# Performance work log

Hardware: AMD Instinct MI355X
Metric: run time of the kernel (lower is better)

## Reference

```python
import jax, jax.numpy as jnp
import numpy as np

N, E, F_IN, H, C = 50000, 800000, 50, 128, 121


def setup_inputs() -> dict:
    key = jax.random.key(0)
    ks = jax.random.split(key, 16)
    s = 0.05
    inp = {
        'x': jax.random.normal(ks[0], (N, F_IN), jnp.float32),
        'edge_index': jax.random.randint(ks[1], (2, E), 0, N, jnp.int64),
        'TRAIN': 0,
        'W1': jax.random.normal(ks[2], (F_IN, H), jnp.float32) * s,
        'b1': jnp.zeros((H,), jnp.float32),
        'W2': jax.random.normal(ks[3], (H, H), jnp.float32) * s,
        'b2': jnp.zeros((H,), jnp.float32),
        'W3': jax.random.normal(ks[4], (H, H), jnp.float32) * s,
        'b3': jnp.zeros((H,), jnp.float32),
        'fcW1': jax.random.normal(ks[5], (H, H), jnp.float32) * s,
        'fcb1': jnp.zeros((H,), jnp.float32),
        'fcW2': jax.random.normal(ks[6], (H, H), jnp.float32) * s,
        'fcb2': jnp.zeros((H,), jnp.float32),
        'fcW3': jax.random.normal(ks[7], (H, C), jnp.float32) * s,
        'fcb3': jnp.zeros((C,), jnp.float32),
    }
    return inp


def gcn_conv(x, W, b, src, dst, n):
    # PyG GCNConv: h = x @ W; symmetric norm with self-loops; aggregate at dst.
    h = x @ W
    deg = jax.ops.segment_sum(jnp.ones(src.shape[0], h.dtype), dst, num_segments=n) + 1.0
    dinv = jax.lax.rsqrt(deg)  # deg^{-1/2}, self-loop included
    norm = dinv[src] * dinv[dst]  # [E]
    agg = jax.ops.segment_sum(h[src] * norm[:, None], dst, num_segments=n)
    agg = agg + h * (dinv * dinv)[:, None]  # self-loop contribution
    return agg + b


def reference(x, edge_index, TRAIN, W1, b1, W2, b2, W3, b3, fcW1, fcb1, fcW2, fcb2, fcW3, fcb3):
    src, dst = edge_index[0], edge_index[1]
    n = x.shape[0]
    y = jax.nn.relu(gcn_conv(x, W1, b1, src, dst, n))
    y = jax.nn.relu(gcn_conv(y, W2, b2, src, dst, n))
    y = jax.nn.relu(gcn_conv(y, W3, b3, src, dst, n))
    y = jax.nn.relu(y @ fcW1 + fcb1)
    y = jax.nn.relu(y @ fcW2 + fcb2)
    y = y @ fcW3 + fcb3
    return y
```

## Files before the change

### kernel.cpp

```cpp
#include <hip/hip_runtime.h>

#define SCAN_CHUNK 2048

typedef short s16x8 __attribute__((ext_vector_type(8)));
typedef float f32x4 __attribute__((ext_vector_type(4)));

__device__ inline ushort f2b(float f) {
  uint u = __float_as_uint(f);
  return (ushort)((u + 0x7fffu + ((u >> 16) & 1u)) >> 16);
}
__device__ inline float b2f(uint h) { return __uint_as_float(h << 16); }

__global__ __launch_bounds__(256) void convert_hist_kernel(const void* __restrict__ ei,
                                                           int* __restrict__ src,
                                                           int* __restrict__ dst,
                                                           int* __restrict__ degi, int E) {
  __shared__ int sflag;
  if (threadIdx.x == 0) {
    const int* p32 = (const int*)ei;
    int is64 = 1;
#pragma unroll 4
    for (int i = 1; i < 256; i += 2)
      if (p32[i] != 0) { is64 = 0; break; }
    sflag = is64;
  }
  __syncthreads();
  int e = blockIdx.x * 256 + threadIdx.x;
  if (e >= E) return;
  int s, d;
  if (sflag) {
    const long long* p = (const long long*)ei;
    s = (int)p[e];
    d = (int)p[E + e];
  } else {
    const int* p = (const int*)ei;
    s = p[e];
    d = p[E + e];
  }
  src[e] = s;
  dst[e] = d;
  atomicAdd(&degi[d], 1);
}

__global__ __launch_bounds__(256) void chunk_reduce_kernel(const int* __restrict__ degi,
                                                           int* __restrict__ partials, int N) {
  __shared__ int s[256];
  int base = blockIdx.x * SCAN_CHUNK;
  int sum = 0;
  for (int j = 0; j < 8; ++j) {
    int i = base + threadIdx.x * 8 + j;
    if (i < N) sum += degi[i];
  }
  s[threadIdx.x] = sum;
  __syncthreads();
  for (int ofs = 128; ofs > 0; ofs >>= 1) {
    if ((int)threadIdx.x < ofs) s[threadIdx.x] += s[threadIdx.x + ofs];
    __syncthreads();
  }
  if (threadIdx.x == 0) partials[blockIdx.x] = s[0];
}

__global__ __launch_bounds__(256) void chunk_scan_kernel(int* __restrict__ degi,
                                                         const int* __restrict__ partials,
                                                         int nchunk,
                                                         int* __restrict__ rowptr,
                                                         float* __restrict__ dinv,
                                                         int N, int E) {
  __shared__ int s[256];
  __shared__ int sbase;
  int t = threadIdx.x;
  if (t == 0) {
    int acc = 0;
    for (int c = 0; c < (int)blockIdx.x; ++c) acc += partials[c];
    sbase = acc;
    if (blockIdx.x == 0) rowptr[N] = E;
  }
  int base = blockIdx.x * SCAN_CHUNK;
  int v[8];
  int tsum = 0;
  for (int j = 0; j < 8; ++j) {
    int i = base + t * 8 + j;
    v[j] = (i < N) ? degi[i] : 0;
    tsum += v[j];
  }
  s[t] = tsum;
  __syncthreads();
  for (int ofs = 1; ofs < 256; ofs <<= 1) {
    int add = (t >= ofs) ? s[t - ofs] : 0;
    __syncthreads();
    s[t] += add;
    __syncthreads();
  }
  int run = s[t] - tsum + sbase;
  for (int j = 0; j < 8; ++j) {
    int i = base + t * 8 + j;
    if (i < N) {
      rowptr[i] = run;
      dinv[i] = rsqrtf((float)v[j] + 1.0f);
      degi[i] = 0;
    }
    run += v[j];
  }
}

__global__ __launch_bounds__(256) void scatter_kernel(const int* __restrict__ src,
                                                      const int* __restrict__ dst,
                                                      const int* __restrict__ rowptr,
                                                      const float* __restrict__ dinv,
                                                      int* __restrict__ cnt,
                                                      uint* __restrict__ epack, int E, int N) {
  const int chunk = blockIdx.x & 7;
  const int group = blockIdx.x >> 3;
  const int ngroup = gridDim.x >> 3;
  const int c0 = (int)(((long)chunk * N) >> 3);
  const int c1 = (int)(((long)(chunk + 1) * N) >> 3);
  for (int e = group * 256 + threadIdx.x; e < E; e += ngroup * 256) {
    int d = dst[e];
    if (d < c0 || d >= c1) continue;
    int s = src[e];
    int slot = rowptr[d] + atomicAdd(&cnt[d], 1);
    float nm = dinv[s] * dinv[d];
    epack[slot] = (uint)s | ((uint)f2b(nm) << 16);
  }
}

__global__ __launch_bounds__(256) void prep_all(const float* __restrict__ W1,
                                                const float* __restrict__ W2,
                                                const float* __restrict__ W3,
                                                const float* __restrict__ F1,
                                                const float* __restrict__ F2,
                                                const float* __restrict__ F3,
                                                const float* __restrict__ x,
                                                ushort* __restrict__ W1t, ushort* __restrict__ W2t,
                                                ushort* __restrict__ W3t, ushort* __restrict__ F1t,
                                                ushort* __restrict__ F2t, ushort* __restrict__ F3t,
                                                ushort* __restrict__ xb, int N) {
  int b = blockIdx.x;
  if (b < 384) {
    int wi = b >> 6;
    int i = (b & 63) * 256 + threadIdx.x;
    const float* W;
    ushort* Wt;
    int K, Kp, ncol;
    switch (wi) {
      case 0: W = W1; Wt = W1t; K = 50; Kp = 64; ncol = 128; break;
      case 1: W = W2; Wt = W2t; K = 128; Kp = 128; ncol = 128; break;
      case 2: W = W3; Wt = W3t; K = 128; Kp = 128; ncol = 128; break;
      case 3: W = F1; Wt = F1t; K = 128; Kp = 128; ncol = 128; break;
      case 4: W = F2; Wt = F2t; K = 128; Kp = 128; ncol = 128; break;
      default: W = F3; Wt = F3t; K = 128; Kp = 128; ncol = 121; break;
    }
    if (i >= 128 * Kp) return;
    int c = i / Kp, k = i - c * Kp;
    float w = (k < K && c < ncol) ? W[(size_t)k * ncol + c] : 0.f;
    Wt[(size_t)c * Kp + k] = f2b(w);
  } else {
    long i = (long)(b - 384) * 256 + threadIdx.x;
    if (i >= (long)N * 64) return;
    int n = (int)(i >> 6), k = (int)(i & 63);
    xb[i] = (k < 50) ? f2b(x[(size_t)n * 50 + k]) : (ushort)0;
  }
}

template <int KSTEPS, bool BIAS, bool RELU>
__global__ __launch_bounds__(256) void mm_mfma(const ushort* __restrict__ X,
                                               const ushort* __restrict__ Wt,
                                               const float* __restrict__ bias,
                                               ushort* __restrict__ Yb, int N) {
  constexpr int K = KSTEPS * 32;
  const int lane = threadIdx.x & 63;
  const int wq = threadIdx.x >> 6;
  const int am = lane & 15;
  const int ag = lane >> 4;

  s16x8 wf[KSTEPS][2];
#pragma unroll
  for (int ks = 0; ks < KSTEPS; ++ks)
#pragma unroll
    for (int f = 0; f < 2; ++f)
      wf[ks][f] = *(const s16x8*)(Wt + (size_t)(wq * 32 + f * 16 + am) * K + ag * 8 + ks * 32);
  float bv[2] = {0.f, 0.f};
  if (BIAS) {
    bv[0] = bias[wq * 32 + am];
    bv[1] = bias[wq * 32 + 16 + am];
  }

  const int ntile = (N + 31) >> 5;
  for (int t = blockIdx.x; t < ntile; t += gridDim.x) {
    const long r0 = (long)t * 32;
    const bool v1 = (r0 + 16) < N;
    const ushort* x0 = X + (size_t)(r0 + am) * K + ag * 8;
    f32x4 acc[2][2] = {};
#pragma unroll
    for (int ks = 0; ks < KSTEPS; ++ks) {
      s16x8 a0 = *(const s16x8*)(x0 + ks * 32);
      s16x8 a1 = {};
      if (v1) a1 = *(const s16x8*)(x0 + (size_t)16 * K + ks * 32);
#pragma unroll
      for (int f = 0; f < 2; ++f) {
        acc[0][f] = __builtin_amdgcn_mfma_f32_16x16x32_bf16(a0, wf[ks][f], acc[0][f], 0, 0, 0);
        if (v1)
          acc[1][f] = __builtin_amdgcn_mfma_f32_16x16x32_bf16(a1, wf[ks][f], acc[1][f], 0, 0, 0);
      }
    }
#pragma unroll
    for (int m = 0; m < 2; ++m) {
      if (m == 1 && !v1) break;
#pragma unroll
      for (int f = 0; f < 2; ++f) {
        int col = wq * 32 + f * 16 + am;
#pragma unroll
        for (int r = 0; r < 4; ++r) {
          long row = r0 + m * 16 + ag * 4 + r;
          float v = acc[m][f][r] + bv[f];
          if (RELU) v = fmaxf(v, 0.f);
          Yb[row * 128 + col] = f2b(v);
        }
      }
    }
  }
}

__global__ __launch_bounds__(256) void fc_fused(const ushort* __restrict__ X,
                                                const ushort* __restrict__ F1t,
                                                const ushort* __restrict__ F2t,
                                                const ushort* __restrict__ F3t,
                                                const float* __restrict__ b1,
                                                const float* __restrict__ b2,
                                                const float* __restrict__ b3,
                                                float* __restrict__ out, int N) {
  __shared__ ushort lds[32 * 128];
  const int lane = threadIdx.x & 63;
  const int wq = threadIdx.x >> 6;
  const int am = lane & 15;
  const int ag = lane >> 4;
  char* my = (char*)lds;

  s16x8 wf1[4][2], wf2[4][2], wf3[4][2];
#pragma unroll
  for (int ks = 0; ks < 4; ++ks)
#pragma unroll
    for (int f = 0; f < 2; ++f) {
      size_t o = (size_t)(wq * 32 + f * 16 + am) * 128 + ag * 8 + ks * 32;
      wf1[ks][f] = *(const s16x8*)(F1t + o);
      wf2[ks][f] = *(const s16x8*)(F2t + o);
      wf3[ks][f] = *(const s16x8*)(F3t + o);
    }
  float b1v[2] = {b1[wq * 32 + am], b1[wq * 32 + 16 + am]};
  float b2v[2] = {b2[wq * 32 + am], b2[wq * 32 + 16 + am]};
  int c0 = wq * 32 + am, c1 = wq * 32 + 16 + am;
  float b3v[2] = {(c0 < 121) ? b3[c0] : 0.f, (c1 < 121) ? b3[c1] : 0.f};

  auto stage = [&](f32x4 acc[2][2], const float* bv) {
#pragma unroll
    for (int m = 0; m < 2; ++m)
#pragma unroll
      for (int f = 0; f < 2; ++f) {
        int col = wq * 32 + f * 16 + am;
#pragma unroll
        for (int r = 0; r < 4; ++r) {
          int row = m * 16 + ag * 4 + r;
          uint byte = (uint)(row * 256 + col * 2) ^ ((uint)(row & 7) << 4);
          *(ushort*)(my + byte) = f2b(fmaxf(acc[m][f][r] + bv[f], 0.f));
        }
      }
  };
  auto loadA = [&](int m, int ks) -> s16x8 {
    int row = m * 16 + am;
    uint byte = (uint)(row * 256 + ks * 64 + ag * 16) ^ ((uint)(row & 7) << 4);
    return *(const s16x8*)(my + byte);
  };

  const int ntile = (N + 31) >> 5;
  for (int t = blockIdx.x; t < ntile; t += gridDim.x) {
    const long r0 = (long)t * 32;
    const bool v1 = (r0 + 16) < N;
    const ushort* x0 = X + (size_t)(r0 + am) * 128 + ag * 8;

    f32x4 a1c[2][2] = {};
#pragma unroll
    for (int ks = 0; ks < 4; ++ks) {
      s16x8 a0 = *(const s16x8*)(x0 + ks * 32);
      s16x8 a1 = v1 ? *(const s16x8*)(x0 + (size_t)16 * 128 + ks * 32) : s16x8{};
#pragma unroll
      for (int f = 0; f < 2; ++f) {
        a1c[0][f] = __builtin_amdgcn_mfma_f32_16x16x32_bf16(a0, wf1[ks][f], a1c[0][f], 0, 0, 0);
        a1c[1][f] = __builtin_amdgcn_mfma_f32_16x16x32_bf16(a1, wf1[ks][f], a1c[1][f], 0, 0, 0);
      }
    }
    stage(a1c, b1v);
    __syncthreads();
    f32x4 a2c[2][2] = {};
#pragma unroll
    for (int ks = 0; ks < 4; ++ks) {
      s16x8 a0 = loadA(0, ks);
      s16x8 a1 = loadA(1, ks);
#pragma unroll
      for (int f = 0; f < 2; ++f) {
        a2c[0][f] = __builtin_amdgcn_mfma_f32_16x16x32_bf16(a0, wf2[ks][f], a2c[0][f], 0, 0, 0);
        a2c[1][f] = __builtin_amdgcn_mfma_f32_16x16x32_bf16(a1, wf2[ks][f], a2c[1][f], 0, 0, 0);
      }
    }
    __syncthreads();
    stage(a2c, b2v);
    __syncthreads();
    f32x4 a3c[2][2] = {};
#pragma unroll
    for (int ks = 0; ks < 4; ++ks) {
      s16x8 a0 = loadA(0, ks);
      s16x8 a1 = loadA(1, ks);
#pragma unroll
      for (int f = 0; f < 2; ++f) {
        a3c[0][f] = __builtin_amdgcn_mfma_f32_16x16x32_bf16(a0, wf3[ks][f], a3c[0][f], 0, 0, 0);
        a3c[1][f] = __builtin_amdgcn_mfma_f32_16x16x32_bf16(a1, wf3[ks][f], a3c[1][f], 0, 0, 0);
      }
    }
#pragma unroll
    for (int m = 0; m < 2; ++m) {
      if (m == 1 && !v1) break;
#pragma unroll
      for (int f = 0; f < 2; ++f) {
        int col = wq * 32 + f * 16 + am;
        if (col >= 121) continue;
#pragma unroll
        for (int r = 0; r < 4; ++r) {
          long row = r0 + m * 16 + ag * 4 + r;
          out[row * 121 + col] = a3c[m][f][r] + b3v[f];
        }
      }
    }
    __syncthreads();
  }
}

template <int RW, bool ACT>
__global__ __launch_bounds__(256) void agg_kernel(const ushort* __restrict__ Hm,
                                                  const int* __restrict__ rowptr,
                                                  const uint* __restrict__ epack,
                                                  const float* __restrict__ dinv,
                                                  const float* __restrict__ b,
                                                  ushort* __restrict__ Y, int N) {
  int wave = threadIdx.x >> 6;
  int lane = threadIdx.x & 63;
  int n = blockIdx.x * 4 + wave;
  if (n >= N) return;
  int beg = rowptr[n], end = rowptr[n + 1];
  float dn = dinv[n];
  float d2 = dn * dn;
  int i = beg;

  if constexpr (RW == 128) {
    int f = lane * 2;
    float ax = 0.f, ay = 0.f;
    while (i + 8 <= end) {
      uint rec[8];
#pragma unroll
      for (int j = 0; j < 8; ++j) rec[j] = epack[i + j];
      uint v[8];
#pragma unroll
      for (int j = 0; j < 8; ++j)
        v[j] = *(const uint*)&Hm[(size_t)(rec[j] & 0xffffu) * 128 + f];
#pragma unroll
      for (int j = 0; j < 8; ++j) {
        float nm = __uint_as_float(rec[j] & 0xffff0000u);
        ax += b2f(v[j] & 0xffffu) * nm;
        ay += b2f(v[j] >> 16) * nm;
      }
      i += 8;
    }
    if (i + 4 <= end) {
      uint rec[4];
#pragma unroll
      for (int j = 0; j < 4; ++j) rec[j] = epack[i + j];
      uint v[4];
#pragma unroll
      for (int j = 0; j < 4; ++j)
        v[j] = *(const uint*)&Hm[(size_t)(rec[j] & 0xffffu) * 128 + f];
#pragma unroll
      for (int j = 0; j < 4; ++j) {
        float nm = __uint_as_float(rec[j] & 0xffff0000u);
        ax += b2f(v[j] & 0xffffu) * nm;
        ay += b2f(v[j] >> 16) * nm;
      }
      i += 4;
    }
    for (; i < end; ++i) {
      uint rec = epack[i];
      float nm = __uint_as_float(rec & 0xffff0000u);
      uint v = *(const uint*)&Hm[(size_t)(rec & 0xffffu) * 128 + f];
      ax += b2f(v & 0xffffu) * nm;
      ay += b2f(v >> 16) * nm;
    }
    uint sv = *(const uint*)&Hm[(size_t)n * 128 + f];
    ax += b2f(sv & 0xffffu) * d2;
    ay += b2f(sv >> 16) * d2;
    if (ACT) {
      ax = fmaxf(ax + b[f], 0.f);
      ay = fmaxf(ay + b[f + 1], 0.f);
    }
    uint out = (uint)f2b(ax) | ((uint)f2b(ay) << 16);
    *(uint*)&Y[(size_t)n * 128 + f] = out;
  } else {
    int f = lane;
    float ax = 0.f;
    while (i + 8 <= end) {
      uint rec[8];
#pragma unroll
      for (int j = 0; j < 8; ++j) rec[j] = epack[i + j];
      ushort v[8];
#pragma unroll
      for (int j = 0; j < 8; ++j)
        v[j] = Hm[(size_t)(rec[j] & 0xffffu) * 64 + f];
#pragma unroll
      for (int j = 0; j < 8; ++j)
        ax += b2f(v[j]) * __uint_as_float(rec[j] & 0xffff0000u);
      i += 8;
    }
    if (i + 4 <= end) {
      uint rec[4];
#pragma unroll
      for (int j = 0; j < 4; ++j) rec[j] = epack[i + j];
      ushort v[4];
#pragma unroll
      for (int j = 0; j < 4; ++j)
        v[j] = Hm[(size_t)(rec[j] & 0xffffu) * 64 + f];
#pragma unroll
      for (int j = 0; j < 4; ++j)
        ax += b2f(v[j]) * __uint_as_float(rec[j] & 0xffff0000u);
      i += 4;
    }
    for (; i < end; ++i) {
      uint rec = epack[i];
      ax += b2f(Hm[(size_t)(rec & 0xffffu) * 64 + f]) * __uint_as_float(rec & 0xffff0000u);
    }
    ax += b2f(Hm[(size_t)n * 64 + f]) * d2;
    if (ACT) ax = fmaxf(ax + b[f], 0.f);
    Y[(size_t)n * 64 + f] = f2b(ax);
  }
}

extern "C" void kernel_launch(void* const* d_in, const int* in_sizes, int n_in,
                              void* d_out, int out_size, void* d_ws, size_t ws_size,
                              hipStream_t stream) {
  const float* x    = (const float*)d_in[0];
  const void*  ei   = d_in[1];
  const float* W1   = (const float*)d_in[3];
  const float* b1   = (const float*)d_in[4];
  const float* W2   = (const float*)d_in[5];
  const float* b2   = (const float*)d_in[6];
  const float* W3   = (const float*)d_in[7];
  const float* b3   = (const float*)d_in[8];
  const float* fcW1 = (const float*)d_in[9];
  const float* fcb1 = (const float*)d_in[10];
  const float* fcW2 = (const float*)d_in[11];
  const float* fcb2 = (const float*)d_in[12];
  const float* fcW3 = (const float*)d_in[13];
  const float* fcb3 = (const float*)d_in[14];

  const int FIN = 50;
  const int N = in_sizes[0] / FIN;
  const int E = in_sizes[1] / 2;
  const int NCHUNK = (N + SCAN_CHUNK - 1) / SCAN_CHUNK;

  size_t off = 0;
  auto carve = [&](size_t bytes) {
    void* p = (char*)d_ws + off;
    off += (bytes + 255) & ~(size_t)255;
    return p;
  };
  int*    src32    = (int*)carve((size_t)E * 4);
  int*    dst32    = (int*)carve((size_t)E * 4);
  uint*   epack    = (uint*)carve((size_t)E * 4);
  int*    degi     = (int*)carve((size_t)N * 4);
  int*    rowptr   = (int*)carve((size_t)(N + 1) * 4);
  float*  dinv     = (float*)carve((size_t)N * 4);
  int*    partials = (int*)carve((size_t)NCHUNK * 4);
  ushort* W1t      = (ushort*)carve((size_t)128 * 64 * 2);
  ushort* W2t      = (ushort*)carve((size_t)128 * 128 * 2);
  ushort* W3t      = (ushort*)carve((size_t)128 * 128 * 2);
  ushort* F1t      = (ushort*)carve((size_t)128 * 128 * 2);
  ushort* F2t      = (ushort*)carve((size_t)128 * 128 * 2);
  ushort* F3t      = (ushort*)carve((size_t)128 * 128 * 2);
  ushort* xb       = (ushort*)carve((size_t)N * 64 * 2);
  ushort* aggX     = (ushort*)carve((size_t)N * 64 * 2);
  ushort* bufA     = (ushort*)carve((size_t)N * 128 * 2);
  ushort* bufB     = (ushort*)carve((size_t)N * 128 * 2);

  const int gE = (E + 255) / 256;
  const int gMM = 1024;
  const int gAGG = (N + 3) / 4;
  const int gPREP = 384 + (int)(((long)N * 64 + 255) / 256);

  hipMemsetAsync(degi, 0, (size_t)N * 4, stream);
  convert_hist_kernel<<<gE, 256, 0, stream>>>(ei, src32, dst32, degi, E);
  chunk_reduce_kernel<<<NCHUNK, 256, 0, stream>>>(degi, partials, N);
  chunk_scan_kernel<<<NCHUNK, 256, 0, stream>>>(degi, partials, NCHUNK, rowptr, dinv, N, E);
  scatter_kernel<<<1024, 256, 0, stream>>>(src32, dst32, rowptr, dinv, degi, epack, E, N);
  prep_all<<<gPREP, 256, 0, stream>>>(W1, W2, W3, fcW1, fcW2, fcW3, x,
                                      W1t, W2t, W3t, F1t, F2t, F3t, xb, N);

  agg_kernel<64, false><<<gAGG, 256, 0, stream>>>(xb, rowptr, epack, dinv, nullptr, aggX, N);
  mm_mfma<2, true, true><<<gMM, 256, 0, stream>>>(aggX, W1t, b1, bufA, N);
  mm_mfma<4, false, false><<<gMM, 256, 0, stream>>>(bufA, W2t, nullptr, bufB, N);
  agg_kernel<128, true><<<gAGG, 256, 0, stream>>>(bufB, rowptr, epack, dinv, b2, bufA, N);
  mm_mfma<4, false, false><<<gMM, 256, 0, stream>>>(bufA, W3t, nullptr, bufB, N);
  agg_kernel<128, true><<<gAGG, 256, 0, stream>>>(bufB, rowptr, epack, dinv, b3, bufA, N);
  fc_fused<<<gMM, 256, 0, stream>>>(bufA, F1t, F2t, F3t, fcb1, fcb2, fcb3,
                                    (float*)d_out, N);
}
```

Before: 259.8 us.

## Fuse prep into convert kernel, drop scan reduce pass, fuse first two matmuls

Merges edge conversion/histogram with weight and feature bf16 prep into one launch. Replaces the separate chunk-reduce kernel by having each scan block sum its own prefix of degrees directly. Fuses the layer-1 matmul (with bias+relu) and the layer-2 matmul into one kernel that keeps the intermediate 32x128 tile in swizzled LDS, avoiding a full N x 128 bf16 round trip through global memory. The scan prefix recompute is quadratic in chunk count but small here; the fused kernel adds LDS sync per tile.

```diff
diff --git a/kernel.cpp b/kernel.cpp
--- a/kernel.cpp
+++ b/kernel.cpp
@@ -11,71 +11,92 @@
 }
 __device__ inline float b2f(uint h) { return __uint_as_float(h << 16); }
 
-__global__ __launch_bounds__(256) void convert_hist_kernel(const void* __restrict__ ei,
-                                                           int* __restrict__ src,
-                                                           int* __restrict__ dst,
-                                                           int* __restrict__ degi, int E) {
-  __shared__ int sflag;
-  if (threadIdx.x == 0) {
-    const int* p32 = (const int*)ei;
-    int is64 = 1;
+__global__ __launch_bounds__(256) void convert_prep(const void* __restrict__ ei,
+                                                    int* __restrict__ src,
+                                                    int* __restrict__ dst,
+                                                    int* __restrict__ degi, int E,
+                                                    const float* __restrict__ W1,
+                                                    const float* __restrict__ W2,
+                                                    const float* __restrict__ W3,
+                                                    const float* __restrict__ F1,
+                                                    const float* __restrict__ F2,
+                                                    const float* __restrict__ F3,
+                                                    const float* __restrict__ x,
+                                                    ushort* __restrict__ W1t, ushort* __restrict__ W2t,
+                                                    ushort* __restrict__ W3t, ushort* __restrict__ F1t,
+                                                    ushort* __restrict__ F2t, ushort* __restrict__ F3t,
+                                                    ushort* __restrict__ xb, int N) {
+  const int gE = (E + 255) / 256;
+  int b = blockIdx.x;
+  if (b < gE) {
+    __shared__ int sflag;
+    if (threadIdx.x == 0) {
+      const int* p32 = (const int*)ei;
+      int is64 = 1;
 #pragma unroll 4
-    for (int i = 1; i < 256; i += 2)
-      if (p32[i] != 0) { is64 = 0; break; }
-    sflag = is64;
-  }
-  __syncthreads();
-  int e = blockIdx.x * 256 + threadIdx.x;
-  if (e >= E) return;
-  int s, d;
-  if (sflag) {
-    const long long* p = (const long long*)ei;
-    s = (int)p[e];
-    d = (int)p[E + e];
+      for (int i = 1; i < 256; i += 2)
+        if (p32[i] != 0) { is64 = 0; break; }
+      sflag = is64;
+    }
+    __syncthreads();
+    int e = b * 256 + threadIdx.x;
+    if (e >= E) return;
+    int s, d;
+    if (sflag) {
+      const long long* p = (const long long*)ei;
+      s = (int)p[e];
+      d = (int)p[E + e];
+    } else {
+      const int* p = (const int*)ei;
+      s = p[e];
+      d = p[E + e];
+    }
+    src[e] = s;
+    dst[e] = d;
+    atomicAdd(&degi[d], 1);
+  } else if (b < gE + 384) {
+    int wi = (b - gE) >> 6;
+    int i = ((b - gE) & 63) * 256 + threadIdx.x;
+    const float* W;
+    ushort* Wt;
+    int K, Kp, ncol;
+    switch (wi) {
+      case 0: W = W1; Wt = W1t; K = 50; Kp = 64; ncol = 128; break;
+      case 1: W = W2; Wt = W2t; K = 128; Kp = 128; ncol = 128; break;
+      case 2: W = W3; Wt = W3t; K = 128; Kp = 128; ncol = 128; break;
+      case 3: W = F1; Wt = F1t; K = 128; Kp = 128; ncol = 128; break;
+      case 4: W = F2; Wt = F2t; K = 128; Kp = 128; ncol = 128; break;
+      default: W = F3; Wt = F3t; K = 128; Kp = 128; ncol = 121; break;
+    }
+    if (i >= 128 * Kp) return;
+    int c = i / Kp, k = i - c * Kp;
+    float w = (k < K && c < ncol) ? W[(size_t)k * ncol + c] : 0.f;
+    Wt[(size_t)c * Kp + k] = f2b(w);
   } else {
-    const int* p = (const int*)ei;
-    s = p[e];
-    d = p[E + e];
-  }
-  src[e] = s;
-  dst[e] = d;
-  atomicAdd(&degi[d], 1);
-}
-
-__global__ __launch_bounds__(256) void chunk_reduce_kernel(const int* __restrict__ degi,
-                                                           int* __restrict__ partials, int N) {
-  __shared__ int s[256];
-  int base = blockIdx.x * SCAN_CHUNK;
-  int sum = 0;
-  for (int j = 0; j < 8; ++j) {
-    int i = base + threadIdx.x * 8 + j;
-    if (i < N) sum += degi[i];
-  }
-  s[threadIdx.x] = sum;
-  __syncthreads();
-  for (int ofs = 128; ofs > 0; ofs >>= 1) {
-    if ((int)threadIdx.x < ofs) s[threadIdx.x] += s[threadIdx.x + ofs];
-    __syncthreads();
-  }
-  if (threadIdx.x == 0) partials[blockIdx.x] = s[0];
+    long i = (long)(b - gE - 384) * 256 + threadIdx.x;
+    if (i >= (long)N * 64) return;
+    int n = (int)(i >> 6), k = (int)(i & 63);
+    xb[i] = (k < 50) ? f2b(x[(size_t)n * 50 + k]) : (ushort)0;
+  }
 }
 
 __global__ __launch_bounds__(256) void chunk_scan_kernel(int* __restrict__ degi,
-                                                         const int* __restrict__ partials,
-                                                         int nchunk,
                                                          int* __restrict__ rowptr,
                                                          float* __restrict__ dinv,
                                                          int N, int E) {
   __shared__ int s[256];
-  __shared__ int sbase;
   int t = threadIdx.x;
-  if (t == 0) {
-    int acc = 0;
-    for (int c = 0; c < (int)blockIdx.x; ++c) acc += partials[c];
-    sbase = acc;
-    if (blockIdx.x == 0) rowptr[N] = E;
-  }
-  int base = blockIdx.x * SCAN_CHUNK;
+  const int base = blockIdx.x * SCAN_CHUNK;
+  int psum = 0;
+  for (int i = t; i < base; i += 256) psum += degi[i];
+  s[t] = psum;
+  __syncthreads();
+  for (int ofs = 128; ofs > 0; ofs >>= 1) {
+    if (t < ofs) s[t] += s[t + ofs];
+    __syncthreads();
+  }
+  int sbase = s[0];
+  __syncthreads();
   int v[8];
   int tsum = 0;
   for (int j = 0; j < 8; ++j) {
@@ -101,6 +122,7 @@
     }
     run += v[j];
   }
+  if (blockIdx.x == 0 && t == 0) rowptr[N] = E;
 }
 
 __global__ __launch_bounds__(256) void scatter_kernel(const int* __restrict__ src,
@@ -124,41 +146,90 @@
   }
 }
 
-__global__ __launch_bounds__(256) void prep_all(const float* __restrict__ W1,
-                                                const float* __restrict__ W2,
-                                                const float* __restrict__ W3,
-                                                const float* __restrict__ F1,
-                                                const float* __restrict__ F2,
-                                                const float* __restrict__ F3,
-                                                const float* __restrict__ x,
-                                                ushort* __restrict__ W1t, ushort* __restrict__ W2t,
-                                                ushort* __restrict__ W3t, ushort* __restrict__ F1t,
-                                                ushort* __restrict__ F2t, ushort* __restrict__ F3t,
-                                                ushort* __restrict__ xb, int N) {
-  int b = blockIdx.x;
-  if (b < 384) {
-    int wi = b >> 6;
-    int i = (b & 63) * 256 + threadIdx.x;
-    const float* W;
-    ushort* Wt;
-    int K, Kp, ncol;
-    switch (wi) {
-      case 0: W = W1; Wt = W1t; K = 50; Kp = 64; ncol = 128; break;
-      case 1: W = W2; Wt = W2t; K = 128; Kp = 128; ncol = 128; break;
-      case 2: W = W3; Wt = W3t; K = 128; Kp = 128; ncol = 128; break;
-      case 3: W = F1; Wt = F1t; K = 128; Kp = 128; ncol = 128; break;
-      case 4: W = F2; Wt = F2t; K = 128; Kp = 128; ncol = 128; break;
-      default: W = F3; Wt = F3t; K = 128; Kp = 128; ncol = 121; break;
-    }
-    if (i >= 128 * Kp) return;
-    int c = i / Kp, k = i - c * Kp;
-    float w = (k < K && c < ncol) ? W[(size_t)k * ncol + c] : 0.f;
-    Wt[(size_t)c * Kp + k] = f2b(w);
-  } else {
-    long i = (long)(b - 384) * 256 + threadIdx.x;
-    if (i >= (long)N * 64) return;
-    int n = (int)(i >> 6), k = (int)(i & 63);
-    xb[i] = (k < 50) ? f2b(x[(size_t)n * 50 + k]) : (ushort)0;
+__global__ __launch_bounds__(256) void mm12_fused(const ushort* __restrict__ X,
+                                                  const ushort* __restrict__ W1t,
+                                                  const ushort* __restrict__ W2t,
+                                                  const float* __restrict__ b1,
+                                                  ushort* __restrict__ Yb, int N) {
+  __shared__ char lds[8192];
+  const int lane = threadIdx.x & 63;
+  const int wq = threadIdx.x >> 6;
+  const int am = lane & 15, ag = lane >> 4;
+
+  s16x8 wf1[2][2], wf2[4][2];
+#pragma unroll
+  for (int ks = 0; ks < 2; ++ks)
+#pragma unroll
+    for (int f = 0; f < 2; ++f)
+      wf1[ks][f] = *(const s16x8*)(W1t + (size_t)(wq * 32 + f * 16 + am) * 64 + ks * 32 + ag * 8);
+#pragma unroll
+  for (int ks = 0; ks < 4; ++ks)
+#pragma unroll
+    for (int f = 0; f < 2; ++f)
+      wf2[ks][f] = *(const s16x8*)(W2t + (size_t)(wq * 32 + f * 16 + am) * 128 + ks * 32 + ag * 8);
+  float b1v[2] = {b1[wq * 32 + am], b1[wq * 32 + 16 + am]};
+
+  auto loadA = [&](int m, int ks) -> s16x8 {
+    int row = m * 16 + am;
+    uint byte = (uint)(row * 256 + ks * 64 + ag * 16) ^ ((uint)(row & 7) << 4);
+    return *(const s16x8*)(lds + byte);
+  };
+
+  const int ntile = (N + 31) >> 5;
+  for (int t = blockIdx.x; t < ntile; t += gridDim.x) {
+    const long r0 = (long)t * 32;
+    const bool v1 = (r0 + 16) < N;
+    const ushort* x0 = X + (size_t)(r0 + am) * 64 + ag * 8;
+
+    f32x4 a1c[2][2] = {};
+#pragma unroll
+    for (int ks = 0; ks < 2; ++ks) {
+      s16x8 a0 = *(const s16x8*)(x0 + ks * 32);
+      s16x8 a1 = v1 ? *(const s16x8*)(x0 + (size_t)16 * 64 + ks * 32) : s16x8{};
+#pragma unroll
+      for (int f = 0; f < 2; ++f) {
+        a1c[0][f] = __builtin_amdgcn_mfma_f32_16x16x32_bf16(a0, wf1[ks][f], a1c[0][f], 0, 0, 0);
+        a1c[1][f] = __builtin_amdgcn_mfma_f32_16x16x32_bf16(a1, wf1[ks][f], a1c[1][f], 0, 0, 0);
+      }
+    }
+#pragma unroll
+    for (int m = 0; m < 2; ++m)
+#pragma unroll
+      for (int f = 0; f < 2; ++f) {
+        int col = wq * 32 + f * 16 + am;
+#pragma unroll
+        for (int r = 0; r < 4; ++r) {
+          int row = m * 16 + ag * 4 + r;
+          uint byte = (uint)(row * 256 + col * 2) ^ ((uint)(row & 7) << 4);
+          *(ushort*)(lds + byte) = f2b(fmaxf(a1c[m][f][r] + b1v[f], 0.f));
+        }
+      }
+    __syncthreads();
+    f32x4 a2c[2][2] = {};
+#pragma unroll
+    for (int ks = 0; ks < 4; ++ks) {
+      s16x8 a0 = loadA(0, ks);
+      s16x8 a1 = loadA(1, ks);
+#pragma unroll
+      for (int f = 0; f < 2; ++f) {
+        a2c[0][f] = __builtin_amdgcn_mfma_f32_16x16x32_bf16(a0, wf2[ks][f], a2c[0][f], 0, 0, 0);
+        a2c[1][f] = __builtin_amdgcn_mfma_f32_16x16x32_bf16(a1, wf2[ks][f], a2c[1][f], 0, 0, 0);
+      }
+    }
+#pragma unroll
+    for (int m = 0; m < 2; ++m) {
+      if (m == 1 && !v1) break;
+#pragma unroll
+      for (int f = 0; f < 2; ++f) {
+        int col = wq * 32 + f * 16 + am;
+#pragma unroll
+        for (int r = 0; r < 4; ++r) {
+          long row = r0 + m * 16 + ag * 4 + r;
+          Yb[row * 128 + col] = f2b(a2c[m][f][r]);
+        }
+      }
+    }
+    __syncthreads();
   }
 }
 
@@ -209,10 +280,11 @@
 #pragma unroll
       for (int f = 0; f < 2; ++f) {
         int col = wq * 32 + f * 16 + am;
+        float bvv = BIAS ? bv[f] : 0.f;
 #pragma unroll
         for (int r = 0; r < 4; ++r) {
           long row = r0 + m * 16 + ag * 4 + r;
-          float v = acc[m][f][r] + bv[f];
+          float v = acc[m][f][r] + bvv;
           if (RELU) v = fmaxf(v, 0.f);
           Yb[row * 128 + col] = f2b(v);
         }
@@ -471,10 +543,9 @@
   int*    src32    = (int*)carve((size_t)E * 4);
   int*    dst32    = (int*)carve((size_t)E * 4);
   uint*   epack    = (uint*)carve((size_t)E * 4);
-  int*    degi     = (int*)carve((size_t)N * 4);
+  int*    degi     = (int*)carve((size_t)(N + 4) * 4);
   int*    rowptr   = (int*)carve((size_t)(N + 1) * 4);
   float*  dinv     = (float*)carve((size_t)N * 4);
-  int*    partials = (int*)carve((size_t)NCHUNK * 4);
   ushort* W1t      = (ushort*)carve((size_t)128 * 64 * 2);
   ushort* W2t      = (ushort*)carve((size_t)128 * 128 * 2);
   ushort* W3t      = (ushort*)carve((size_t)128 * 128 * 2);
@@ -487,21 +558,19 @@
   ushort* bufB     = (ushort*)carve((size_t)N * 128 * 2);
 
   const int gE = (E + 255) / 256;
+  const int gXB = (int)(((long)N * 64 + 255) / 256);
   const int gMM = 1024;
   const int gAGG = (N + 3) / 4;
-  const int gPREP = 384 + (int)(((long)N * 64 + 255) / 256);
 
   hipMemsetAsync(degi, 0, (size_t)N * 4, stream);
-  convert_hist_kernel<<<gE, 256, 0, stream>>>(ei, src32, dst32, degi, E);
-  chunk_reduce_kernel<<<NCHUNK, 256, 0, stream>>>(degi, partials, N);
-  chunk_scan_kernel<<<NCHUNK, 256, 0, stream>>>(degi, partials, NCHUNK, rowptr, dinv, N, E);
+  convert_prep<<<gE + 384 + gXB, 256, 0, stream>>>(ei, src32, dst32, degi, E,
+                                                   W1, W2, W3, fcW1, fcW2, fcW3, x,
+                                                   W1t, W2t, W3t, F1t, F2t, F3t, xb, N);
+  chunk_scan_kernel<<<NCHUNK, 256, 0, stream>>>(degi, rowptr, dinv, N, E);
   scatter_kernel<<<1024, 256, 0, stream>>>(src32, dst32, rowptr, dinv, degi, epack, E, N);
-  prep_all<<<gPREP, 256, 0, stream>>>(W1, W2, W3, fcW1, fcW2, fcW3, x,
-                                      W1t, W2t, W3t, F1t, F2t, F3t, xb, N);
 
   agg_kernel<64, false><<<gAGG, 256, 0, stream>>>(xb, rowptr, epack, dinv, nullptr, aggX, N);
-  mm_mfma<2, true, true><<<gMM, 256, 0, stream>>>(aggX, W1t, b1, bufA, N);
-  mm_mfma<4, false, false><<<gMM, 256, 0, stream>>>(bufA, W2t, nullptr, bufB, N);
+  mm12_fused<<<gMM, 256, 0, stream>>>(aggX, W1t, W2t, b1, bufB, N);
   agg_kernel<128, true><<<gAGG, 256, 0, stream>>>(bufB, rowptr, epack, dinv, b2, bufA, N);
   mm_mfma<4, false, false><<<gMM, 256, 0, stream>>>(bufA, W3t, nullptr, bufB, N);
   agg_kernel<128, true><<<gAGG, 256, 0, stream>>>(bufB, rowptr, epack, dinv, b3, bufA, N);
```

Result: slower. 268.4 us (+3.3%).
